# Optimization experiments

Hardware: AMD Instinct MI355X
Metric: run time of the kernel (lower is better)

Reference implementation:

```python
import jax, jax.numpy as jnp
import numpy as np

C = 256          # input_dim
OUT = 256        # output_dim
DM = C // 4      # mamba d_model
DS = 16          # d_state
DC = 4           # d_conv
DI = 2 * DM      # d_inner (expand=2)
DTR = max(1, -(-DM // 16))  # dt_rank = ceil(d_model/16) = 4
B, Dd, H, W = 2, 8, 16, 32


def setup_inputs() -> dict:
    key = jax.random.key(0)
    ks = jax.random.split(key, 12)
    s = 0.02
    inp = {
        'x': jax.random.normal(ks[0], (B, C, Dd, H, W), jnp.float32),
        'ln_g': jnp.ones((C,), jnp.float32),
        'ln_b': jnp.zeros((C,), jnp.float32),
        'in_proj_w': jax.random.normal(ks[1], (2 * DI, DM), jnp.float32) * s,
        'conv_w': jax.random.normal(ks[2], (DI, DC), jnp.float32) * s,
        'conv_b': jnp.zeros((DI,), jnp.float32),
        'x_proj_w': jax.random.normal(ks[3], (DTR + 2 * DS, DI), jnp.float32) * s,
        'dt_proj_w': jax.random.normal(ks[4], (DI, DTR), jnp.float32) * s,
        'dt_proj_b': jax.random.uniform(ks[5], (DI,), jnp.float32, -4.0, -2.0),
        'A_log': jnp.log(jnp.broadcast_to(jnp.arange(1, DS + 1, dtype=jnp.float32), (DI, DS))),
        'D_param': jnp.ones((DI,), jnp.float32),
        'out_proj_w': jax.random.normal(ks[6], (DM, DI), jnp.float32) * s,
        'proj_w': jax.random.normal(ks[7], (OUT, C), jnp.float32) * s,
        'proj_b': jnp.zeros((OUT,), jnp.float32),
        'skip_scale': jnp.ones((1,), jnp.float32),
    }
    return inp


def _layernorm(h, g, b, eps=1e-5):
    mu = jnp.mean(h, axis=-1, keepdims=True)
    var = jnp.mean(jnp.square(h - mu), axis=-1, keepdims=True)
    return (h - mu) * jax.lax.rsqrt(var + eps) * g + b


def _mamba(xp, in_proj_w, conv_w, conv_b, x_proj_w, dt_proj_w, dt_proj_b, A_log, D_param, out_proj_w):
    # xp: (B, L, DM)
    xz = xp @ in_proj_w.T                      # (B, L, 2*DI)
    xc, z = jnp.split(xz, 2, axis=-1)
    # causal depthwise conv1d, kernel DC, left-pad DC-1
    xcT = xc.transpose(0, 2, 1)                # (B, DI, L)
    k = conv_w[:, None, :]                     # (DI, 1, DC)
    conv = jax.lax.conv_general_dilated(xcT, k, (1,), [(DC - 1, 0)], feature_group_count=DI)
    xc = jax.nn.silu(conv + conv_b[None, :, None]).transpose(0, 2, 1)  # (B, L, DI)
    x_dbl = xc @ x_proj_w.T                    # (B, L, DTR+2*DS)
    dt = x_dbl[..., :DTR]
    Bm = x_dbl[..., DTR:DTR + DS]
    Cm = x_dbl[..., DTR + DS:]
    dt = jax.nn.softplus(dt @ dt_proj_w.T + dt_proj_b)  # (B, L, DI)
    A = -jnp.exp(A_log)                        # (DI, DS)
    dA = jnp.exp(dt[..., None] * A)            # (B, L, DI, DS)
    dBx = dt[..., None] * Bm[:, :, None, :] * xc[..., None]  # (B, L, DI, DS)

    def step(h, inp):
        dA_t, dBx_t, C_t = inp
        h = dA_t * h + dBx_t                   # (B, DI, DS)
        y = jnp.einsum('bds,bs->bd', h, C_t)
        return h, y

    h0 = jnp.zeros((xp.shape[0], DI, DS), xp.dtype)
    _, ys = jax.lax.scan(step, h0, (dA.transpose(1, 0, 2, 3), dBx.transpose(1, 0, 2, 3), Cm.transpose(1, 0, 2)))
    y = ys.transpose(1, 0, 2) + D_param * xc   # (B, L, DI)
    y = y * jax.nn.silu(z)
    return y @ out_proj_w.T                    # (B, L, DM)


def reference(x, ln_g, ln_b, in_proj_w, conv_w, conv_b, x_proj_w, dt_proj_w, dt_proj_b,
              A_log, D_param, out_proj_w, proj_w, proj_b, skip_scale):
    Bb, Cc, Dd_, H_, W_ = x.shape
    L = Dd_ * H_ * W_
    xf = x.reshape(Bb, Cc, L).transpose(0, 2, 1)        # (B, L, C)
    xn = _layernorm(xf, ln_g, ln_b)
    parts = xn.reshape(Bb, L, 4, DM).transpose(2, 0, 1, 3)  # (4, B, L, DM), contiguous chunks
    mam = lambda p: _mamba(p, in_proj_w, conv_w, conv_b, x_proj_w, dt_proj_w,
                           dt_proj_b, A_log, D_param, out_proj_w)
    outs = jax.vmap(mam)(parts) + skip_scale * parts    # shared Mamba weights across chunks
    xm = outs.transpose(1, 2, 0, 3).reshape(Bb, L, Cc)
    xm = _layernorm(xm, ln_g, ln_b)                      # same LN module reused
    xp = (xm @ proj_w.T + proj_b).transpose(0, 2, 1)     # (B, OUT, L)
    return xp.reshape(Bb, -1, Dd_, H_, W_)
```

## Files before the change

kernel.cpp:

```cpp
#include <hip/hip_runtime.h>


#define B_    2
#define C_    256
#define L_    4096
#define P_    4
#define DM_   64
#define DI_   128
#define OUT_  256
#define NCH   128
#define CHL   32

__global__ __launch_bounds__(256) void k1_ln(const float* __restrict__ x,
        const float* __restrict__ g, const float* __restrict__ bb,
        float* __restrict__ xn) {
  __shared__ float tile[256][33];
  __shared__ float psum[8][32];
  __shared__ float psq[8][32];
  __shared__ float smu[32], srs[32];
  int t = threadIdx.x;
  int l0 = blockIdx.x * 32;
  int b = blockIdx.y;
  const float* xb = x + (size_t)b * C_ * L_;
  int ll = t & 31, cr = t >> 5;
  for (int i = 0; i < 32; ++i) {
    int c = cr + 8 * i;
    tile[c][ll] = xb[(size_t)c * L_ + l0 + ll];
  }
  __syncthreads();
  {
    int l = t & 31, k = t >> 5;
    float s = 0.f, sq = 0.f;
    #pragma unroll 8
    for (int j = 0; j < 32; ++j) {
      float v = tile[32 * k + j][l];
      s += v; sq += v * v;
    }
    psum[k][l] = s; psq[k][l] = sq;
  }
  __syncthreads();
  if (t < 32) {
    float s = 0.f, sq = 0.f;
    #pragma unroll
    for (int k = 0; k < 8; ++k) { s += psum[k][t]; sq += psq[k][t]; }
    float mu = s * (1.f / 256.f);
    float var = sq * (1.f / 256.f) - mu * mu;
    smu[t] = mu;
    srs[t] = rsqrtf(var + 1e-5f);
  }
  __syncthreads();
  float gc = g[t], bc = bb[t];
  for (int l = 0; l < 32; ++l) {
    float v = (tile[t][l] - smu[l]) * srs[l] * gc + bc;
    xn[((size_t)b * L_ + l0 + l) * C_ + t] = v;
  }
}

__global__ __launch_bounds__(256) void k2_inproj(const float* __restrict__ xn,
        const float* __restrict__ w, float* __restrict__ xz) {
  __shared__ float sa[64 * 64];
  int t = threadIdx.x;
  int row0 = blockIdx.x * 64;
  int o0 = blockIdx.y * 32;
  int bp = row0 >> 12, b = bp >> 2, p = bp & 3, l0 = row0 & 4095;
  #pragma unroll
  for (int i = 0; i < 4; ++i) {
    int idx = t + 256 * i;
    int row = idx >> 4, kq = idx & 15;
    float4 v = *(const float4*)&xn[((size_t)b * L_ + l0 + row) * 256 + p * 64 + kq * 4];
    *(float4*)&sa[row * 64 + ((kq ^ (row & 15)) << 2)] = v;
  }
  __syncthreads();
  int lane = t & 63;
  int wid = __builtin_amdgcn_readfirstlane(t >> 6);
  int ob = o0 + wid * 8;
  const float* wp0 = w + (size_t)ob * 64;
  float acc[8];
  #pragma unroll
  for (int c = 0; c < 8; ++c) acc[c] = 0.f;
  #pragma unroll 2
  for (int k4 = 0; k4 < 16; ++k4) {
    float4 a4 = *(const float4*)&sa[lane * 64 + ((k4 ^ (lane & 15)) << 2)];
    #pragma unroll
    for (int c = 0; c < 8; ++c) {
      float4 w4 = *(const float4*)&wp0[c * 64 + k4 * 4];
      acc[c] += a4.x * w4.x + a4.y * w4.y + a4.z * w4.z + a4.w * w4.w;
    }
  }
  __syncthreads();
  int widl = t >> 6;
  #pragma unroll
  for (int c = 0; c < 8; ++c) sa[lane * 33 + widl * 8 + c] = acc[c];
  __syncthreads();
  {
    int row = t >> 2, c0 = (t & 3) * 8;
    float4 v0 = *(const float4*)&sa[row * 33 + c0];
    float4 v1 = *(const float4*)&sa[row * 33 + c0 + 4];
    float* op = &xz[(size_t)(row0 + row) * 256 + o0 + c0];
    *(float4*)op = v0;
    *(float4*)&op[4] = v1;
  }
}

__global__ __launch_bounds__(256) void k3a_conv(const float* __restrict__ xz,
        const float* __restrict__ conv_w, const float* __restrict__ conv_b,
        float* __restrict__ xc) {
  int t = threadIdx.x;
  int d = t & 127, lh = t >> 7;
  int bp = blockIdx.y;
  int lstart = blockIdx.x * 32 + lh * 16;
  const float* xzb = xz + (size_t)bp * L_ * 256;
  float4 cw = *(const float4*)&conv_w[d * 4];
  float cb = conv_b[d];
  float w0 = (lstart >= 3) ? xzb[(size_t)(lstart - 3) * 256 + d] : 0.f;
  float w1 = (lstart >= 2) ? xzb[(size_t)(lstart - 2) * 256 + d] : 0.f;
  float w2 = (lstart >= 1) ? xzb[(size_t)(lstart - 1) * 256 + d] : 0.f;
  const float* xzrow = xzb + (size_t)lstart * 256 + d;
  float* xcrow = xc + ((size_t)bp * L_ + lstart) * 128 + d;
  #pragma unroll 4
  for (int i = 0; i < 16; ++i) {
    float w3 = xzrow[(size_t)i * 256];
    float cv = cb + cw.x * w0 + cw.y * w1 + cw.z * w2 + cw.w * w3;
    float sv = __fdividef(cv, 1.f + __expf(-cv));
    xcrow[(size_t)i * 128] = sv;
    w0 = w1; w1 = w2; w2 = w3;
  }
}

__global__ __launch_bounds__(256) void k3b_xdbl(const float* __restrict__ xc,
        const float* __restrict__ x_proj_w, const float* __restrict__ dt_proj_w,
        const float* __restrict__ dt_proj_b,
        float* __restrict__ bc, float* __restrict__ dt) {
  __shared__ float sa[64 * 64];
  __shared__ float sbc[64 * 33];
  __shared__ float sdb[64 * 8];
  int t = threadIdx.x;
  int row0 = blockIdx.x * 64;
  int lane = t & 63;
  int wid = __builtin_amdgcn_readfirstlane(t >> 6);
  const float* wbase = x_proj_w + (size_t)(wid * 9) * 128;
  float acc[9];
  #pragma unroll
  for (int rr = 0; rr < 9; ++rr) acc[rr] = 0.f;
  for (int kt = 0; kt < 2; ++kt) {
    if (kt) __syncthreads();
    #pragma unroll
    for (int i = 0; i < 4; ++i) {
      int idx = t + 256 * i;
      int row = idx >> 4, kq = idx & 15;
      float4 v = *(const float4*)&xc[(size_t)(row0 + row) * 128 + kt * 64 + kq * 4];
      *(float4*)&sa[row * 64 + ((kq ^ (row & 15)) << 2)] = v;
    }
    __syncthreads();
    #pragma unroll 2
    for (int k4 = 0; k4 < 16; ++k4) {
      float4 a4 = *(const float4*)&sa[lane * 64 + ((k4 ^ (lane & 15)) << 2)];
      #pragma unroll
      for (int rr = 0; rr < 9; ++rr) {
        float4 w4 = *(const float4*)&wbase[rr * 128 + kt * 64 + k4 * 4];
        acc[rr] += a4.x * w4.x + a4.y * w4.y + a4.z * w4.z + a4.w * w4.w;
      }
    }
  }
  if (wid == 0) {
    #pragma unroll
    for (int rr = 0; rr < 4; ++rr) sdb[lane * 8 + rr] = acc[rr];
    #pragma unroll
    for (int rr = 4; rr < 9; ++rr) sbc[lane * 33 + (rr - 4)] = acc[rr];
  } else {
    #pragma unroll
    for (int rr = 0; rr < 9; ++rr) sbc[lane * 33 + (wid * 9 + rr - 4)] = acc[rr];
  }
  __syncthreads();
  #pragma unroll
  for (int i = 0; i < 8; ++i) {
    int idx = t + 256 * i;
    int row = idx >> 5, col = idx & 31;
    bc[(size_t)(row0 + row) * 32 + col] = sbc[row * 33 + col];
  }
  {
    int d = t & 127, rh = t >> 7;
    float4 dw = *(const float4*)&dt_proj_w[d * 4];
    float dpb = dt_proj_b[d];
    #pragma unroll 4
    for (int i = 0; i < 32; ++i) {
      int row = rh * 32 + i;
      float4 q = *(const float4*)&sdb[row * 8];
      float v = dpb + q.x * dw.x + q.y * dw.y + q.z * dw.z + q.w * dw.w;
      float sp = (v > 20.f) ? v : __logf(1.f + __expf(v));
      dt[(size_t)(row0 + row) * 128 + d] = sp;
    }
  }
}

__global__ __launch_bounds__(128) void k4a_scanA(const float* __restrict__ dt,
        const float* __restrict__ xc, const float* __restrict__ bcbuf,
        const float* __restrict__ A_log,
        float* __restrict__ chA, float* __restrict__ chH) {
  int d = threadIdx.x;
  int ch = blockIdx.x, bp = blockIdx.y;
  float Av[16], h[16];
  #pragma unroll
  for (int q = 0; q < 4; ++q) {
    float4 a = *(const float4*)&A_log[d * 16 + q * 4];
    Av[q*4+0] = -__expf(a.x); Av[q*4+1] = -__expf(a.y);
    Av[q*4+2] = -__expf(a.z); Av[q*4+3] = -__expf(a.w);
  }
  #pragma unroll
  for (int s = 0; s < 16; ++s) h[s] = 0.f;
  float sumdt = 0.f;
  const float* dtp = dt + (size_t)bp * L_ * 128 + (size_t)ch * CHL * 128 + d;
  const float* xcp = xc + (size_t)bp * L_ * 128 + (size_t)ch * CHL * 128 + d;
  const float* bcp = bcbuf + (size_t)bp * L_ * 32 + (size_t)ch * CHL * 32;
  #pragma unroll 2
  for (int tt = 0; tt < CHL; ++tt) {
    float dtv = dtp[tt * 128];
    float xcv = xcp[tt * 128];
    float Bv[16];
    *(float4*)&Bv[0]  = *(const float4*)&bcp[tt * 32 + 0];
    *(float4*)&Bv[4]  = *(const float4*)&bcp[tt * 32 + 4];
    *(float4*)&Bv[8]  = *(const float4*)&bcp[tt * 32 + 8];
    *(float4*)&Bv[12] = *(const float4*)&bcp[tt * 32 + 12];
    float w = dtv * xcv;
    sumdt += dtv;
    #pragma unroll
    for (int s = 0; s < 16; ++s) {
      float dA = __expf(dtv * Av[s]);
      h[s] = fmaf(dA, h[s], w * Bv[s]);
    }
  }
  size_t o = (((size_t)bp * NCH + ch) * 128 + d) * 16;
  #pragma unroll
  for (int s = 0; s < 16; ++s) chA[o + s] = __expf(sumdt * Av[s]);
  #pragma unroll
  for (int s = 0; s < 16; ++s) chH[o + s] = h[s];
}

__global__ __launch_bounds__(256) void k4b1(const float* __restrict__ chA,
        const float* __restrict__ chH, float* __restrict__ pA,
        float* __restrict__ pH) {
  int tid = blockIdx.x * 256 + threadIdx.x;
  int rem = tid & 2047, g = (tid >> 11) & 15, bp = tid >> 15;
  float a = 1.f, h = 0.f;
  #pragma unroll 2
  for (int i = 0; i < 8; ++i) {
    size_t o = ((size_t)(bp * NCH + g * 8 + i)) * 2048 + rem;
    float ca = chA[o], ce = chH[o];
    h = fmaf(ca, h, ce);
    a *= ca;
  }
  pA[tid] = a; pH[tid] = h;
}

__global__ __launch_bounds__(256) void k4b2(const float* __restrict__ pA,
        const float* __restrict__ pH, float* __restrict__ gH) {
  int tid = blockIdx.x * 256 + threadIdx.x;
  int rem = tid & 2047, bp = tid >> 11;
  float h = 0.f;
  for (int g = 0; g < 16; ++g) {
    int o = (bp << 15) + (g << 11) + rem;
    gH[o] = h;
    h = fmaf(pA[o], h, pH[o]);
  }
}

__global__ __launch_bounds__(256) void k4b3(const float* __restrict__ chA,
        float* __restrict__ chH, const float* __restrict__ gH) {
  int tid = blockIdx.x * 256 + threadIdx.x;
  int rem = tid & 2047, g = (tid >> 11) & 15, bp = tid >> 15;
  float h = gH[tid];
  #pragma unroll 2
  for (int i = 0; i < 8; ++i) {
    size_t o = ((size_t)(bp * NCH + g * 8 + i)) * 2048 + rem;
    float a = chA[o], e = chH[o];
    chH[o] = h;
    h = fmaf(a, h, e);
  }
}

__global__ __launch_bounds__(128) void k5_scanB(const float* __restrict__ dt,
        const float* __restrict__ xc, const float* __restrict__ bcbuf,
        const float* __restrict__ xz, const float* __restrict__ A_log,
        const float* __restrict__ D_param, const float* __restrict__ chH,
        float* __restrict__ yg) {
  int d = threadIdx.x;
  int ch = blockIdx.x, bp = blockIdx.y;
  float Av[16], h[16];
  #pragma unroll
  for (int q = 0; q < 4; ++q) {
    float4 a = *(const float4*)&A_log[d * 16 + q * 4];
    Av[q*4+0] = -__expf(a.x); Av[q*4+1] = -__expf(a.y);
    Av[q*4+2] = -__expf(a.z); Av[q*4+3] = -__expf(a.w);
  }
  {
    size_t o = (((size_t)bp * NCH + ch) * 128 + d) * 16;
    #pragma unroll
    for (int q = 0; q < 4; ++q)
      *(float4*)&h[q * 4] = *(const float4*)&chH[o + q * 4];
  }
  float Dv = D_param[d];
  const float* dtp = dt + (size_t)bp * L_ * 128 + (size_t)ch * CHL * 128 + d;
  const float* xcp = xc + (size_t)bp * L_ * 128 + (size_t)ch * CHL * 128 + d;
  const float* bcp = bcbuf + (size_t)bp * L_ * 32 + (size_t)ch * CHL * 32;
  const float* zp  = xz + (size_t)bp * L_ * 256 + (size_t)ch * CHL * 256 + 128 + d;
  float* ygp = yg + (size_t)bp * L_ * 128 + (size_t)ch * CHL * 128 + d;
  #pragma unroll 2
  for (int tt = 0; tt < CHL; ++tt) {
    float dtv = dtp[tt * 128];
    float xcv = xcp[tt * 128];
    float zv  = zp[tt * 256];
    float Bv[16], Cv[16];
    *(float4*)&Bv[0]  = *(const float4*)&bcp[tt * 32 + 0];
    *(float4*)&Bv[4]  = *(const float4*)&bcp[tt * 32 + 4];
    *(float4*)&Bv[8]  = *(const float4*)&bcp[tt * 32 + 8];
    *(float4*)&Bv[12] = *(const float4*)&bcp[tt * 32 + 12];
    *(float4*)&Cv[0]  = *(const float4*)&bcp[tt * 32 + 16];
    *(float4*)&Cv[4]  = *(const float4*)&bcp[tt * 32 + 20];
    *(float4*)&Cv[8]  = *(const float4*)&bcp[tt * 32 + 24];
    *(float4*)&Cv[12] = *(const float4*)&bcp[tt * 32 + 28];
    float w = dtv * xcv;
    float r = 0.f;
    #pragma unroll
    for (int s = 0; s < 16; ++s) {
      float dA = __expf(dtv * Av[s]);
      h[s] = fmaf(dA, h[s], w * Bv[s]);
      r = fmaf(h[s], Cv[s], r);
    }
    float y = fmaf(Dv, xcv, r);
    float sig = __fdividef(1.f, 1.f + __expf(-zv));
    ygp[tt * 128] = y * (zv * sig);
  }
}

__global__ __launch_bounds__(256) void k6a_gemm(const float* __restrict__ yg,
        const float* __restrict__ xn, const float* __restrict__ opw,
        const float* __restrict__ skip, float* __restrict__ xmn) {
  __shared__ float sa[64 * 64];
  int t = threadIdx.x;
  int row0 = blockIdx.x * 64;
  int o0 = blockIdx.y * 32;
  int bp = row0 >> 12, b = bp >> 2, p = bp & 3, l0 = row0 & 4095;
  int lane = t & 63;
  int wid = __builtin_amdgcn_readfirstlane(t >> 6);
  int ob = o0 + wid * 8;
  const float* wp0 = opw + (size_t)ob * 128;
  float acc[8];
  #pragma unroll
  for (int c = 0; c < 8; ++c) acc[c] = 0.f;
  for (int kt = 0; kt < 2; ++kt) {
    if (kt) __syncthreads();
    #pragma unroll
    for (int i = 0; i < 4; ++i) {
      int idx = t + 256 * i;
      int row = idx >> 4, kq = idx & 15;
      float4 v = *(const float4*)&yg[(size_t)(row0 + row) * 128 + kt * 64 + kq * 4];
      *(float4*)&sa[row * 64 + ((kq ^ (row & 15)) << 2)] = v;
    }
    __syncthreads();
    #pragma unroll 2
    for (int k4 = 0; k4 < 16; ++k4) {
      float4 a4 = *(const float4*)&sa[lane * 64 + ((k4 ^ (lane & 15)) << 2)];
      #pragma unroll
      for (int c = 0; c < 8; ++c) {
        float4 w4 = *(const float4*)&wp0[c * 128 + kt * 64 + k4 * 4];
        acc[c] += a4.x * w4.x + a4.y * w4.y + a4.z * w4.z + a4.w * w4.w;
      }
    }
  }
  __syncthreads();
  int widl = t >> 6;
  #pragma unroll
  for (int c = 0; c < 8; ++c) sa[lane * 33 + widl * 8 + c] = acc[c];
  __syncthreads();
  {
    float sk = skip[0];
    int row = t >> 2, c0 = (t & 3) * 8;
    size_t addr = ((size_t)b * L_ + l0 + row) * 256 + p * 64 + o0 + c0;
    float4 v0 = *(const float4*)&sa[row * 33 + c0];
    float4 v1 = *(const float4*)&sa[row * 33 + c0 + 4];
    float4 x0 = *(const float4*)&xn[addr];
    float4 x1 = *(const float4*)&xn[addr + 4];
    float4 o0v = make_float4(v0.x + sk * x0.x, v0.y + sk * x0.y,
                             v0.z + sk * x0.z, v0.w + sk * x0.w);
    float4 o1v = make_float4(v1.x + sk * x1.x, v1.y + sk * x1.y,
                             v1.z + sk * x1.z, v1.w + sk * x1.w);
    *(float4*)&xmn[addr] = o0v;
    *(float4*)&xmn[addr + 4] = o1v;
  }
}

__global__ __launch_bounds__(256) void k6ln(float* __restrict__ xmn,
        const float* __restrict__ g, const float* __restrict__ bb) {
  int t = threadIdx.x;
  int row = blockIdx.x * 4 + (t >> 6);
  int lane = t & 63;
  float* rp = xmn + (size_t)row * 256 + lane * 4;
  float4 v = *(const float4*)rp;
  float s = v.x + v.y + v.z + v.w;
  float q = v.x * v.x + v.y * v.y + v.z * v.z + v.w * v.w;
  #pragma unroll
  for (int off = 1; off < 64; off <<= 1) {
    s += __shfl_xor(s, off);
    q += __shfl_xor(q, off);
  }
  float mu = s * (1.f / 256.f);
  float rs = rsqrtf(q * (1.f / 256.f) - mu * mu + 1e-5f);
  float4 g4 = *(const float4*)&g[lane * 4];
  float4 b4 = *(const float4*)&bb[lane * 4];
  float4 o = make_float4((v.x - mu) * rs * g4.x + b4.x,
                         (v.y - mu) * rs * g4.y + b4.y,
                         (v.z - mu) * rs * g4.z + b4.z,
                         (v.w - mu) * rs * g4.w + b4.w);
  *(float4*)rp = o;
}

__global__ __launch_bounds__(256) void k6b_proj(const float* __restrict__ xmn,
        const float* __restrict__ pw, const float* __restrict__ pb,
        float* __restrict__ out) {
  __shared__ float sa[64 * 64];
  int t = threadIdx.x;
  int row0 = blockIdx.x * 64;
  int o0 = blockIdx.y * 32;
  int b = row0 >> 12, l0 = row0 & 4095;
  int lane = t & 63;
  int wid = __builtin_amdgcn_readfirstlane(t >> 6);
  int ob = o0 + wid * 8;
  const float* wp0 = pw + (size_t)ob * 256;
  float acc[8];
  #pragma unroll
  for (int c = 0; c < 8; ++c) acc[c] = 0.f;
  for (int kt = 0; kt < 4; ++kt) {
    if (kt) __syncthreads();
    #pragma unroll
    for (int i = 0; i < 4; ++i) {
      int idx = t + 256 * i;
      int row = idx >> 4, kq = idx & 15;
      float4 v = *(const float4*)&xmn[(size_t)(row0 + row) * 256 + kt * 64 + kq * 4];
      *(float4*)&sa[row * 64 + ((kq ^ (row & 15)) << 2)] = v;
    }
    __syncthreads();
    #pragma unroll 2
    for (int k4 = 0; k4 < 16; ++k4) {
      float4 a4 = *(const float4*)&sa[lane * 64 + ((k4 ^ (lane & 15)) << 2)];
      #pragma unroll
      for (int c = 0; c < 8; ++c) {
        float4 w4 = *(const float4*)&wp0[c * 256 + kt * 64 + k4 * 4];
        acc[c] += a4.x * w4.x + a4.y * w4.y + a4.z * w4.z + a4.w * w4.w;
      }
    }
  }
  #pragma unroll
  for (int c = 0; c < 8; ++c) {
    int o = ob + c;
    out[((size_t)b * OUT_ + o) * L_ + l0 + lane] = acc[c] + pb[o];
  }
}

extern "C" void kernel_launch(void* const* d_in, const int* in_sizes, int n_in,
                              void* d_out, int out_size, void* d_ws, size_t ws_size,
                              hipStream_t stream) {
  (void)in_sizes; (void)n_in; (void)out_size; (void)ws_size;
  const float* x          = (const float*)d_in[0];
  const float* ln_g       = (const float*)d_in[1];
  const float* ln_b       = (const float*)d_in[2];
  const float* in_proj_w  = (const float*)d_in[3];
  const float* conv_w     = (const float*)d_in[4];
  const float* conv_b     = (const float*)d_in[5];
  const float* x_proj_w   = (const float*)d_in[6];
  const float* dt_proj_w  = (const float*)d_in[7];
  const float* dt_proj_b  = (const float*)d_in[8];
  const float* A_log      = (const float*)d_in[9];
  const float* D_param    = (const float*)d_in[10];
  const float* out_proj_w = (const float*)d_in[11];
  const float* proj_w     = (const float*)d_in[12];
  const float* proj_b     = (const float*)d_in[13];
  const float* skip_scale = (const float*)d_in[14];

  float* ws  = (float*)d_ws;
  float* xn  = ws;
  float* xz  = xn + 2097152;
  float* xc  = xz + 8388608;
  float* dt  = xc + 4194304;
  float* bc  = dt + 4194304;
  float* chA = bc + 1048576;
  float* chH = chA + 2097152;
  float* yg  = chH + 2097152;
  float* xmn = yg + 4194304;
  float* pA  = xmn;
  float* pH  = xmn + 262144;
  float* gH  = xmn + 524288;
  float* out = (float*)d_out;

  k1_ln<<<dim3(L_ / 32, B_), 256, 0, stream>>>(x, ln_g, ln_b, xn);
  k2_inproj<<<dim3(512, 8), 256, 0, stream>>>(xn, in_proj_w, xz);
  k3a_conv<<<dim3(128, B_ * P_), 256, 0, stream>>>(xz, conv_w, conv_b, xc);
  k3b_xdbl<<<dim3(512), 256, 0, stream>>>(xc, x_proj_w, dt_proj_w,
      dt_proj_b, bc, dt);
  k4a_scanA<<<dim3(NCH, B_ * P_), 128, 0, stream>>>(dt, xc, bc, A_log, chA, chH);
  k4b1<<<dim3(1024), 256, 0, stream>>>(chA, chH, pA, pH);
  k4b2<<<dim3(64), 256, 0, stream>>>(pA, pH, gH);
  k4b3<<<dim3(1024), 256, 0, stream>>>(chA, chH, gH);
  k5_scanB<<<dim3(NCH, B_ * P_), 128, 0, stream>>>(dt, xc, bc, xz, A_log,
      D_param, chH, yg);
  k6a_gemm<<<dim3(512, 2), 256, 0, stream>>>(yg, xn, out_proj_w, skip_scale, xmn);
  k6ln<<<dim3(B_ * L_ / 4), 256, 0, stream>>>(xmn, ln_g, ln_b);
  k6b_proj<<<dim3(128, 8), 256, 0, stream>>>(xmn, proj_w, proj_b, out);
}
```

Measured before the change: 244.2 us.

## Fuse in_proj, conv, x_proj and dt stages; fuse out_proj with skip and LayerNorm

Merges in-projection, causal depthwise conv with SiLU, x_proj and dt_proj/softplus into one kernel per 64-row tile. The tile keeps xn and the conv input in shared memory, recomputing the three halo rows, so the full xz buffer is never written and read back. The z half is stored already passed through SiLU in a compact buffer, which removes the sigmoid from the scan kernel. The out-projection GEMM now covers all four chunks per row, then adds the skip term and applies LayerNorm in the same kernel, dropping the separate LN pass. The cost is more shared memory and registers per block and fewer blocks, which may reduce occupancy.

```diff
diff --git a/kernel.cpp b/kernel.cpp
--- a/kernel.cpp
+++ b/kernel.cpp
@@ -56,140 +56,170 @@
   }
 }
 
-__global__ __launch_bounds__(256) void k2_inproj(const float* __restrict__ xn,
-        const float* __restrict__ w, float* __restrict__ xz) {
-  __shared__ float sa[64 * 64];
+__global__ __launch_bounds__(256) void k23_fused(const float* __restrict__ xn,
+        const float* __restrict__ ipw, const float* __restrict__ conv_w,
+        const float* __restrict__ conv_b, const float* __restrict__ x_proj_w,
+        const float* __restrict__ dt_proj_w, const float* __restrict__ dt_proj_b,
+        float* __restrict__ xc, float* __restrict__ zs,
+        float* __restrict__ bc, float* __restrict__ dt) {
+  __shared__ float sxn[67 * 64];
+  __shared__ float sxc[67 * 128];
+  __shared__ float sdb[64 * 8];
+  __shared__ float sbc[64 * 33];
   int t = threadIdx.x;
-  int row0 = blockIdx.x * 64;
-  int o0 = blockIdx.y * 32;
-  int bp = row0 >> 12, b = bp >> 2, p = bp & 3, l0 = row0 & 4095;
-  #pragma unroll
-  for (int i = 0; i < 4; ++i) {
+  int l0 = blockIdx.x * 64;
+  int bp = blockIdx.y;
+  int b = bp >> 2, p = bp & 3;
+  for (int i = 0; i < 5; ++i) {
     int idx = t + 256 * i;
-    int row = idx >> 4, kq = idx & 15;
-    float4 v = *(const float4*)&xn[((size_t)b * L_ + l0 + row) * 256 + p * 64 + kq * 4];
-    *(float4*)&sa[row * 64 + ((kq ^ (row & 15)) << 2)] = v;
+    if (idx < 67 * 16) {
+      int r = idx >> 4, kq = idx & 15;
+      int l = l0 - 3 + r;
+      float4 v = make_float4(0.f, 0.f, 0.f, 0.f);
+      if (l >= 0) v = *(const float4*)&xn[((size_t)b * L_ + l) * 256 + p * 64 + kq * 4];
+      *(float4*)&sxn[r * 64 + ((kq ^ (r & 15)) << 2)] = v;
+    }
   }
   __syncthreads();
   int lane = t & 63;
   int wid = __builtin_amdgcn_readfirstlane(t >> 6);
-  int ob = o0 + wid * 8;
-  const float* wp0 = w + (size_t)ob * 64;
-  float acc[8];
-  #pragma unroll
-  for (int c = 0; c < 8; ++c) acc[c] = 0.f;
-  #pragma unroll 2
-  for (int k4 = 0; k4 < 16; ++k4) {
-    float4 a4 = *(const float4*)&sa[lane * 64 + ((k4 ^ (lane & 15)) << 2)];
-    #pragma unroll
-    for (int c = 0; c < 8; ++c) {
-      float4 w4 = *(const float4*)&wp0[c * 64 + k4 * 4];
-      acc[c] += a4.x * w4.x + a4.y * w4.y + a4.z * w4.z + a4.w * w4.w;
-    }
-  }
-  __syncthreads();
-  int widl = t >> 6;
-  #pragma unroll
-  for (int c = 0; c < 8; ++c) sa[lane * 33 + widl * 8 + c] = acc[c];
-  __syncthreads();
+  int rb = lane + 3;
+  for (int ot = 0; ot < 4; ++ot) {
+    int ob = ot * 32 + wid * 8;
+    const float* wp0 = ipw + (size_t)ob * 64;
+    float acc[8];
+    #pragma unroll
+    for (int c = 0; c < 8; ++c) acc[c] = 0.f;
+    for (int k4 = 0; k4 < 16; ++k4) {
+      float4 a4 = *(const float4*)&sxn[rb * 64 + ((k4 ^ (rb & 15)) << 2)];
+      #pragma unroll
+      for (int c = 0; c < 8; ++c) {
+        float4 w4 = *(const float4*)&wp0[c * 64 + k4 * 4];
+        acc[c] += a4.x * w4.x + a4.y * w4.y + a4.z * w4.z + a4.w * w4.w;
+      }
+    }
+    int oq = ob >> 2;
+    *(float4*)&sxc[rb * 128 + (((oq + 0) ^ (rb & 15)) << 2)] =
+        make_float4(acc[0], acc[1], acc[2], acc[3]);
+    *(float4*)&sxc[rb * 128 + (((oq + 1) ^ (rb & 15)) << 2)] =
+        make_float4(acc[4], acc[5], acc[6], acc[7]);
+  }
+  #pragma unroll
+  for (int it = 0; it < 2; ++it) {
+    int idx = t + 256 * it;
+    if (idx < 384) {
+      int r = idx >> 7, o = idx & 127;
+      float a = 0.f;
+      for (int k4 = 0; k4 < 16; ++k4) {
+        float4 a4 = *(const float4*)&sxn[r * 64 + ((k4 ^ r) << 2)];
+        float4 w4 = *(const float4*)&ipw[(size_t)o * 64 + k4 * 4];
+        a += a4.x * w4.x + a4.y * w4.y + a4.z * w4.z + a4.w * w4.w;
+      }
+      sxc[r * 128 + (((o >> 2) ^ r) << 2) + (o & 3)] = a;
+    }
+  }
+  __syncthreads();
+  int d = t & 127, lh = t >> 7;
+  int dq = d >> 2, dl = d & 3;
+  float cv32[32];
   {
-    int row = t >> 2, c0 = (t & 3) * 8;
-    float4 v0 = *(const float4*)&sa[row * 33 + c0];
-    float4 v1 = *(const float4*)&sa[row * 33 + c0 + 4];
-    float* op = &xz[(size_t)(row0 + row) * 256 + o0 + c0];
-    *(float4*)op = v0;
-    *(float4*)&op[4] = v1;
-  }
-}
-
-__global__ __launch_bounds__(256) void k3a_conv(const float* __restrict__ xz,
-        const float* __restrict__ conv_w, const float* __restrict__ conv_b,
-        float* __restrict__ xc) {
-  int t = threadIdx.x;
-  int d = t & 127, lh = t >> 7;
-  int bp = blockIdx.y;
-  int lstart = blockIdx.x * 32 + lh * 16;
-  const float* xzb = xz + (size_t)bp * L_ * 256;
-  float4 cw = *(const float4*)&conv_w[d * 4];
-  float cb = conv_b[d];
-  float w0 = (lstart >= 3) ? xzb[(size_t)(lstart - 3) * 256 + d] : 0.f;
-  float w1 = (lstart >= 2) ? xzb[(size_t)(lstart - 2) * 256 + d] : 0.f;
-  float w2 = (lstart >= 1) ? xzb[(size_t)(lstart - 1) * 256 + d] : 0.f;
-  const float* xzrow = xzb + (size_t)lstart * 256 + d;
-  float* xcrow = xc + ((size_t)bp * L_ + lstart) * 128 + d;
-  #pragma unroll 4
-  for (int i = 0; i < 16; ++i) {
-    float w3 = xzrow[(size_t)i * 256];
-    float cv = cb + cw.x * w0 + cw.y * w1 + cw.z * w2 + cw.w * w3;
-    float sv = __fdividef(cv, 1.f + __expf(-cv));
-    xcrow[(size_t)i * 128] = sv;
-    w0 = w1; w1 = w2; w2 = w3;
-  }
-}
-
-__global__ __launch_bounds__(256) void k3b_xdbl(const float* __restrict__ xc,
-        const float* __restrict__ x_proj_w, const float* __restrict__ dt_proj_w,
-        const float* __restrict__ dt_proj_b,
-        float* __restrict__ bc, float* __restrict__ dt) {
-  __shared__ float sa[64 * 64];
-  __shared__ float sbc[64 * 33];
-  __shared__ float sdb[64 * 8];
-  int t = threadIdx.x;
-  int row0 = blockIdx.x * 64;
-  int lane = t & 63;
-  int wid = __builtin_amdgcn_readfirstlane(t >> 6);
-  const float* wbase = x_proj_w + (size_t)(wid * 9) * 128;
-  float acc[9];
-  #pragma unroll
-  for (int rr = 0; rr < 9; ++rr) acc[rr] = 0.f;
-  for (int kt = 0; kt < 2; ++kt) {
-    if (kt) __syncthreads();
-    #pragma unroll
-    for (int i = 0; i < 4; ++i) {
-      int idx = t + 256 * i;
-      int row = idx >> 4, kq = idx & 15;
-      float4 v = *(const float4*)&xc[(size_t)(row0 + row) * 128 + kt * 64 + kq * 4];
-      *(float4*)&sa[row * 64 + ((kq ^ (row & 15)) << 2)] = v;
-    }
-    __syncthreads();
-    #pragma unroll 2
-    for (int k4 = 0; k4 < 16; ++k4) {
-      float4 a4 = *(const float4*)&sa[lane * 64 + ((k4 ^ (lane & 15)) << 2)];
+    float4 cw = *(const float4*)&conv_w[d * 4];
+    float cb = conv_b[d];
+    int r0 = lh * 32;
+    float w0 = sxc[(r0 + 0) * 128 + ((dq ^ ((r0 + 0) & 15)) << 2) + dl];
+    float w1 = sxc[(r0 + 1) * 128 + ((dq ^ ((r0 + 1) & 15)) << 2) + dl];
+    float w2 = sxc[(r0 + 2) * 128 + ((dq ^ ((r0 + 2) & 15)) << 2) + dl];
+    float* xcp = xc + ((size_t)bp * L_ + l0 + r0) * 128 + d;
+    #pragma unroll
+    for (int i = 0; i < 32; ++i) {
+      int rin = r0 + i + 3;
+      float w3 = sxc[rin * 128 + ((dq ^ (rin & 15)) << 2) + dl];
+      float cvv = cb + cw.x * w0 + cw.y * w1 + cw.z * w2 + cw.w * w3;
+      float sv = __fdividef(cvv, 1.f + __expf(-cvv));
+      cv32[i] = sv;
+      xcp[(size_t)i * 128] = sv;
+      w0 = w1; w1 = w2; w2 = w3;
+    }
+  }
+  __syncthreads();
+  #pragma unroll
+  for (int i = 0; i < 32; ++i) {
+    int rbw = lh * 32 + i + 3;
+    sxc[rbw * 128 + ((dq ^ (rbw & 15)) << 2) + dl] = cv32[i];
+  }
+  __syncthreads();
+  {
+    const float* wbase = x_proj_w + (size_t)(wid * 9) * 128;
+    float acc[9];
+    #pragma unroll
+    for (int rr = 0; rr < 9; ++rr) acc[rr] = 0.f;
+    for (int k4 = 0; k4 < 32; ++k4) {
+      float4 a4 = *(const float4*)&sxc[rb * 128 + ((k4 ^ (rb & 15)) << 2)];
       #pragma unroll
       for (int rr = 0; rr < 9; ++rr) {
-        float4 w4 = *(const float4*)&wbase[rr * 128 + kt * 64 + k4 * 4];
+        float4 w4 = *(const float4*)&wbase[rr * 128 + k4 * 4];
         acc[rr] += a4.x * w4.x + a4.y * w4.y + a4.z * w4.z + a4.w * w4.w;
       }
     }
-  }
-  if (wid == 0) {
-    #pragma unroll
-    for (int rr = 0; rr < 4; ++rr) sdb[lane * 8 + rr] = acc[rr];
-    #pragma unroll
-    for (int rr = 4; rr < 9; ++rr) sbc[lane * 33 + (rr - 4)] = acc[rr];
-  } else {
-    #pragma unroll
-    for (int rr = 0; rr < 9; ++rr) sbc[lane * 33 + (wid * 9 + rr - 4)] = acc[rr];
+    if (wid == 0) {
+      #pragma unroll
+      for (int rr = 0; rr < 4; ++rr) sdb[lane * 8 + rr] = acc[rr];
+      #pragma unroll
+      for (int rr = 4; rr < 9; ++rr) sbc[lane * 33 + (rr - 4)] = acc[rr];
+    } else {
+      #pragma unroll
+      for (int rr = 0; rr < 9; ++rr) sbc[lane * 33 + (wid * 9 + rr - 4)] = acc[rr];
+    }
   }
   __syncthreads();
   #pragma unroll
   for (int i = 0; i < 8; ++i) {
     int idx = t + 256 * i;
     int row = idx >> 5, col = idx & 31;
-    bc[(size_t)(row0 + row) * 32 + col] = sbc[row * 33 + col];
+    bc[((size_t)bp * L_ + l0 + row) * 32 + col] = sbc[row * 33 + col];
   }
   {
-    int d = t & 127, rh = t >> 7;
     float4 dw = *(const float4*)&dt_proj_w[d * 4];
     float dpb = dt_proj_b[d];
     #pragma unroll 4
     for (int i = 0; i < 32; ++i) {
-      int row = rh * 32 + i;
+      int row = lh * 32 + i;
       float4 q = *(const float4*)&sdb[row * 8];
       float v = dpb + q.x * dw.x + q.y * dw.y + q.z * dw.z + q.w * dw.w;
       float sp = (v > 20.f) ? v : __logf(1.f + __expf(v));
-      dt[(size_t)(row0 + row) * 128 + d] = sp;
-    }
+      dt[((size_t)bp * L_ + l0 + row) * 128 + d] = sp;
+    }
+  }
+  for (int ot = 0; ot < 4; ++ot) {
+    int ob = ot * 32 + wid * 8;
+    const float* wp0 = ipw + (size_t)(128 + ob) * 64;
+    float acc[8];
+    #pragma unroll
+    for (int c = 0; c < 8; ++c) acc[c] = 0.f;
+    for (int k4 = 0; k4 < 16; ++k4) {
+      float4 a4 = *(const float4*)&sxn[rb * 64 + ((k4 ^ (rb & 15)) << 2)];
+      #pragma unroll
+      for (int c = 0; c < 8; ++c) {
+        float4 w4 = *(const float4*)&wp0[c * 64 + k4 * 4];
+        acc[c] += a4.x * w4.x + a4.y * w4.y + a4.z * w4.z + a4.w * w4.w;
+      }
+    }
+    #pragma unroll
+    for (int c = 0; c < 8; ++c)
+      acc[c] = __fdividef(acc[c], 1.f + __expf(-acc[c]));
+    int oq = ob >> 2;
+    *(float4*)&sxc[lane * 128 + (((oq + 0) ^ (lane & 15)) << 2)] =
+        make_float4(acc[0], acc[1], acc[2], acc[3]);
+    *(float4*)&sxc[lane * 128 + (((oq + 1) ^ (lane & 15)) << 2)] =
+        make_float4(acc[4], acc[5], acc[6], acc[7]);
+  }
+  __syncthreads();
+  #pragma unroll
+  for (int i = 0; i < 8; ++i) {
+    int idx = t + 256 * i;
+    int row = idx >> 5, cq = idx & 31;
+    float4 v = *(const float4*)&sxc[row * 128 + ((cq ^ (row & 15)) << 2)];
+    *(float4*)&zs[((size_t)bp * L_ + l0 + row) * 128 + cq * 4] = v;
   }
 }
 
@@ -280,7 +310,7 @@
 
 __global__ __launch_bounds__(128) void k5_scanB(const float* __restrict__ dt,
         const float* __restrict__ xc, const float* __restrict__ bcbuf,
-        const float* __restrict__ xz, const float* __restrict__ A_log,
+        const float* __restrict__ zs, const float* __restrict__ A_log,
         const float* __restrict__ D_param, const float* __restrict__ chH,
         float* __restrict__ yg) {
   int d = threadIdx.x;
@@ -302,13 +332,13 @@
   const float* dtp = dt + (size_t)bp * L_ * 128 + (size_t)ch * CHL * 128 + d;
   const float* xcp = xc + (size_t)bp * L_ * 128 + (size_t)ch * CHL * 128 + d;
   const float* bcp = bcbuf + (size_t)bp * L_ * 32 + (size_t)ch * CHL * 32;
-  const float* zp  = xz + (size_t)bp * L_ * 256 + (size_t)ch * CHL * 256 + 128 + d;
+  const float* zp  = zs + (size_t)bp * L_ * 128 + (size_t)ch * CHL * 128 + d;
   float* ygp = yg + (size_t)bp * L_ * 128 + (size_t)ch * CHL * 128 + d;
   #pragma unroll 2
   for (int tt = 0; tt < CHL; ++tt) {
     float dtv = dtp[tt * 128];
     float xcv = xcp[tt * 128];
-    float zv  = zp[tt * 256];
+    float zv  = zp[tt * 128];
     float Bv[16], Cv[16];
     *(float4*)&Bv[0]  = *(const float4*)&bcp[tt * 32 + 0];
     *(float4*)&Bv[4]  = *(const float4*)&bcp[tt * 32 + 4];
@@ -327,91 +357,88 @@
       r = fmaf(h[s], Cv[s], r);
     }
     float y = fmaf(Dv, xcv, r);
-    float sig = __fdividef(1.f, 1.f + __expf(-zv));
-    ygp[tt * 128] = y * (zv * sig);
-  }
-}
-
-__global__ __launch_bounds__(256) void k6a_gemm(const float* __restrict__ yg,
+    ygp[tt * 128] = y * zv;
+  }
+}
+
+__global__ __launch_bounds__(256) void k6a_fused(const float* __restrict__ yg,
         const float* __restrict__ xn, const float* __restrict__ opw,
-        const float* __restrict__ skip, float* __restrict__ xmn) {
-  __shared__ float sa[64 * 64];
+        const float* __restrict__ skip, const float* __restrict__ g,
+        const float* __restrict__ bbias, float* __restrict__ xmn) {
+  __shared__ float syg[2 * 32 * 128];
+  __shared__ float sxm[32 * 256];
   int t = threadIdx.x;
-  int row0 = blockIdx.x * 64;
-  int o0 = blockIdx.y * 32;
-  int bp = row0 >> 12, b = bp >> 2, p = bp & 3, l0 = row0 & 4095;
+  int row0 = blockIdx.x * 32;
+  int b = row0 >> 12, l0 = row0 & 4095;
   int lane = t & 63;
   int wid = __builtin_amdgcn_readfirstlane(t >> 6);
-  int ob = o0 + wid * 8;
-  const float* wp0 = opw + (size_t)ob * 128;
-  float acc[8];
-  #pragma unroll
-  for (int c = 0; c < 8; ++c) acc[c] = 0.f;
-  for (int kt = 0; kt < 2; ++kt) {
-    if (kt) __syncthreads();
-    #pragma unroll
-    for (int i = 0; i < 4; ++i) {
+  int row = lane & 31, ph = lane >> 5;
+  for (int pp = 0; pp < 2; ++pp) {
+    if (pp) __syncthreads();
+    #pragma unroll
+    for (int i = 0; i < 8; ++i) {
       int idx = t + 256 * i;
-      int row = idx >> 4, kq = idx & 15;
-      float4 v = *(const float4*)&yg[(size_t)(row0 + row) * 128 + kt * 64 + kq * 4];
-      *(float4*)&sa[row * 64 + ((kq ^ (row & 15)) << 2)] = v;
+      int part = idx >> 10, rr = (idx >> 5) & 31, cq = idx & 31;
+      float4 v = *(const float4*)&yg[(((size_t)(b * 4 + pp * 2 + part)) * L_ + l0 + rr) * 128 + cq * 4];
+      *(float4*)&syg[part * 4096 + rr * 128 + ((cq ^ (rr & 7)) << 2)] = v;
     }
     __syncthreads();
-    #pragma unroll 2
-    for (int k4 = 0; k4 < 16; ++k4) {
-      float4 a4 = *(const float4*)&sa[lane * 64 + ((k4 ^ (lane & 15)) << 2)];
-      #pragma unroll
-      for (int c = 0; c < 8; ++c) {
-        float4 w4 = *(const float4*)&wp0[c * 128 + kt * 64 + k4 * 4];
-        acc[c] += a4.x * w4.x + a4.y * w4.y + a4.z * w4.z + a4.w * w4.w;
+    for (int ot = 0; ot < 2; ++ot) {
+      int ob = ot * 32 + wid * 8;
+      const float* wp0 = opw + (size_t)ob * 128;
+      float acc[8];
+      #pragma unroll
+      for (int c = 0; c < 8; ++c) acc[c] = 0.f;
+      for (int k4 = 0; k4 < 32; ++k4) {
+        float4 a4 = *(const float4*)&syg[ph * 4096 + row * 128 + ((k4 ^ (row & 7)) << 2)];
+        #pragma unroll
+        for (int c = 0; c < 8; ++c) {
+          float4 w4 = *(const float4*)&wp0[c * 128 + k4 * 4];
+          acc[c] += a4.x * w4.x + a4.y * w4.y + a4.z * w4.z + a4.w * w4.w;
+        }
       }
-    }
-  }
-  __syncthreads();
-  int widl = t >> 6;
-  #pragma unroll
-  for (int c = 0; c < 8; ++c) sa[lane * 33 + widl * 8 + c] = acc[c];
+      int q0 = ((pp * 2 + ph) * 64 + ob) >> 2;
+      *(float4*)&sxm[row * 256 + (((q0 + 0) ^ (row & 7)) << 2)] =
+          make_float4(acc[0], acc[1], acc[2], acc[3]);
+      *(float4*)&sxm[row * 256 + (((q0 + 1) ^ (row & 7)) << 2)] =
+          make_float4(acc[4], acc[5], acc[6], acc[7]);
+    }
+  }
   __syncthreads();
   {
     float sk = skip[0];
-    int row = t >> 2, c0 = (t & 3) * 8;
-    size_t addr = ((size_t)b * L_ + l0 + row) * 256 + p * 64 + o0 + c0;
-    float4 v0 = *(const float4*)&sa[row * 33 + c0];
-    float4 v1 = *(const float4*)&sa[row * 33 + c0 + 4];
-    float4 x0 = *(const float4*)&xn[addr];
-    float4 x1 = *(const float4*)&xn[addr + 4];
-    float4 o0v = make_float4(v0.x + sk * x0.x, v0.y + sk * x0.y,
-                             v0.z + sk * x0.z, v0.w + sk * x0.w);
-    float4 o1v = make_float4(v1.x + sk * x1.x, v1.y + sk * x1.y,
-                             v1.z + sk * x1.z, v1.w + sk * x1.w);
-    *(float4*)&xmn[addr] = o0v;
-    *(float4*)&xmn[addr + 4] = o1v;
-  }
-}
-
-__global__ __launch_bounds__(256) void k6ln(float* __restrict__ xmn,
-        const float* __restrict__ g, const float* __restrict__ bb) {
-  int t = threadIdx.x;
-  int row = blockIdx.x * 4 + (t >> 6);
-  int lane = t & 63;
-  float* rp = xmn + (size_t)row * 256 + lane * 4;
-  float4 v = *(const float4*)rp;
-  float s = v.x + v.y + v.z + v.w;
-  float q = v.x * v.x + v.y * v.y + v.z * v.z + v.w * v.w;
-  #pragma unroll
-  for (int off = 1; off < 64; off <<= 1) {
-    s += __shfl_xor(s, off);
-    q += __shfl_xor(q, off);
-  }
-  float mu = s * (1.f / 256.f);
-  float rs = rsqrtf(q * (1.f / 256.f) - mu * mu + 1e-5f);
-  float4 g4 = *(const float4*)&g[lane * 4];
-  float4 b4 = *(const float4*)&bb[lane * 4];
-  float4 o = make_float4((v.x - mu) * rs * g4.x + b4.x,
-                         (v.y - mu) * rs * g4.y + b4.y,
-                         (v.z - mu) * rs * g4.z + b4.z,
-                         (v.w - mu) * rs * g4.w + b4.w);
-  *(float4*)rp = o;
+    int rowL = t >> 3, cg = t & 7;
+    const float* xnp = xn + ((size_t)b * L_ + l0 + rowL) * 256 + cg * 32;
+    float4 v4[8];
+    float s = 0.f, q = 0.f;
+    #pragma unroll
+    for (int k = 0; k < 8; ++k) {
+      int qq = cg * 8 + k;
+      float4 mv = *(const float4*)&sxm[rowL * 256 + ((qq ^ (rowL & 7)) << 2)];
+      float4 xv = *(const float4*)&xnp[k * 4];
+      mv.x += sk * xv.x; mv.y += sk * xv.y; mv.z += sk * xv.z; mv.w += sk * xv.w;
+      v4[k] = mv;
+      s += mv.x + mv.y + mv.z + mv.w;
+      q += mv.x * mv.x + mv.y * mv.y + mv.z * mv.z + mv.w * mv.w;
+    }
+    s += __shfl_xor(s, 1); q += __shfl_xor(q, 1);
+    s += __shfl_xor(s, 2); q += __shfl_xor(q, 2);
+    s += __shfl_xor(s, 4); q += __shfl_xor(q, 4);
+    float mu = s * (1.f / 256.f);
+    float rs = rsqrtf(q * (1.f / 256.f) - mu * mu + 1e-5f);
+    float* op = &xmn[((size_t)b * L_ + l0 + rowL) * 256 + cg * 32];
+    #pragma unroll
+    for (int k = 0; k < 8; ++k) {
+      float4 g4 = *(const float4*)&g[cg * 32 + k * 4];
+      float4 b4 = *(const float4*)&bbias[cg * 32 + k * 4];
+      float4 mv = v4[k];
+      float4 ov = make_float4((mv.x - mu) * rs * g4.x + b4.x,
+                              (mv.y - mu) * rs * g4.y + b4.y,
+                              (mv.z - mu) * rs * g4.z + b4.z,
+                              (mv.w - mu) * rs * g4.w + b4.w);
+      *(float4*)&op[k * 4] = ov;
+    }
+  }
 }
 
 __global__ __launch_bounds__(256) void k6b_proj(const float* __restrict__ xmn,
@@ -478,8 +505,8 @@
 
   float* ws  = (float*)d_ws;
   float* xn  = ws;
-  float* xz  = xn + 2097152;
-  float* xc  = xz + 8388608;
+  float* zs  = xn + 2097152;
+  float* xc  = zs + 4194304;
   float* dt  = xc + 4194304;
   float* bc  = dt + 4194304;
   float* chA = bc + 1048576;
@@ -492,17 +519,15 @@
   float* out = (float*)d_out;
 
   k1_ln<<<dim3(L_ / 32, B_), 256, 0, stream>>>(x, ln_g, ln_b, xn);
-  k2_inproj<<<dim3(512, 8), 256, 0, stream>>>(xn, in_proj_w, xz);
-  k3a_conv<<<dim3(128, B_ * P_), 256, 0, stream>>>(xz, conv_w, conv_b, xc);
-  k3b_xdbl<<<dim3(512), 256, 0, stream>>>(xc, x_proj_w, dt_proj_w,
-      dt_proj_b, bc, dt);
+  k23_fused<<<dim3(L_ / 64, B_ * P_), 256, 0, stream>>>(xn, in_proj_w, conv_w,
+      conv_b, x_proj_w, dt_proj_w, dt_proj_b, xc, zs, bc, dt);
   k4a_scanA<<<dim3(NCH, B_ * P_), 128, 0, stream>>>(dt, xc, bc, A_log, chA, chH);
   k4b1<<<dim3(1024), 256, 0, stream>>>(chA, chH, pA, pH);
   k4b2<<<dim3(64), 256, 0, stream>>>(pA, pH, gH);
   k4b3<<<dim3(1024), 256, 0, stream>>>(chA, chH, gH);
-  k5_scanB<<<dim3(NCH, B_ * P_), 128, 0, stream>>>(dt, xc, bc, xz, A_log,
+  k5_scanB<<<dim3(NCH, B_ * P_), 128, 0, stream>>>(dt, xc, bc, zs, A_log,
       D_param, chH, yg);
-  k6a_gemm<<<dim3(512, 2), 256, 0, stream>>>(yg, xn, out_proj_w, skip_scale, xmn);
-  k6ln<<<dim3(B_ * L_ / 4), 256, 0, stream>>>(xmn, ln_g, ln_b);
+  k6a_fused<<<dim3(256), 256, 0, stream>>>(yg, xn, out_proj_w, skip_scale,
+      ln_g, ln_b, xmn);
   k6b_proj<<<dim3(128, 8), 256, 0, stream>>>(xmn, proj_w, proj_b, out);
 }
```

After: 278.8 us. 14.2% more time.
